# Optimization experiments

Hardware: AMD Instinct MI355X
Metric: run time of the kernel (lower is better)

Reference implementation:

```python
import jax, jax.numpy as jnp
import numpy as np

B, D, N, M = 32, 512, 1024, 1024

def setup_inputs() -> dict:
    key = jax.random.key(0)
    k1, k2 = jax.random.split(key)
    embedding_1 = jax.random.normal(k1, (B, D, N), dtype=jnp.float32)
    embedding_2 = jax.random.normal(k2, (B, D, M), dtype=jnp.float32)
    return {"embedding_1": embedding_1, "embedding_2": embedding_2}

def reference(embedding_1, embedding_2):
    # att[b, n, m] = sum_d e1[b, d, n] * e2[b, d, m]   (bmm of e1^T with e2)
    att = jnp.einsum('bdn,bdm->bnm', embedding_1, embedding_2)
    # double max-pool: max over m then over n -> global max of score matrix
    s = jnp.max(att, axis=(-1, -2))  # [B]
    return s[:, None]  # [B, 1]
```

## Files before the change

### kernel.cpp

```cpp
#include <hip/hip_runtime.h>
#include <hip/hip_bf16.h>

#define B_ 32
#define D_ 512
#define N_ 1024
#define M_ 1024
#define BT 256
#define BK 64
#define NSTEP (D_ / BK)

typedef __attribute__((ext_vector_type(8))) short bf16x8;
typedef __attribute__((ext_vector_type(4))) short s16x4;
typedef __attribute__((ext_vector_type(4))) float f32x4;
typedef __attribute__((ext_vector_type(4))) int   i32x4;
typedef unsigned short ushort_t;

__device__ __forceinline__ unsigned map_f(float f) {
    unsigned b = __float_as_uint(f);
    return (b & 0x80000000u) ? ~b : (b | 0x80000000u);
}

struct __align__(16) GSmem {
    ushort_t As[2][BT * BK];
    ushort_t Bs[2][BT * BK];
    float red[8];
};

__device__ __forceinline__ void load_tile(const float* __restrict__ p, int k0,
                                          int krb, int gr, float4* fl) {
    #pragma unroll
    for (int it = 0; it < 4; ++it) {
        const float* q = p + (size_t)(k0 + krb + it) * N_ + gr * 8;
        fl[2 * it]     = *reinterpret_cast<const float4*>(q);
        fl[2 * it + 1] = *reinterpret_cast<const float4*>(q + 4);
    }
}

__device__ __forceinline__ void flush_tile(char* lds, int krb, int gr, const float4* fl) {
    #pragma unroll
    for (int it = 0; it < 4; ++it) {
        const int k = krb + it;
        const float4& f0 = fl[2 * it];
        const float4& f1 = fl[2 * it + 1];
        __hip_bfloat162 h0 = __float22bfloat162_rn(make_float2(f0.x, f0.y));
        __hip_bfloat162 h1 = __float22bfloat162_rn(make_float2(f0.z, f0.w));
        __hip_bfloat162 h2 = __float22bfloat162_rn(make_float2(f1.x, f1.y));
        __hip_bfloat162 h3 = __float22bfloat162_rn(make_float2(f1.z, f1.w));
        i32x4 v = { *reinterpret_cast<const int*>(&h0), *reinterpret_cast<const int*>(&h1),
                    *reinterpret_cast<const int*>(&h2), *reinterpret_cast<const int*>(&h3) };
        *reinterpret_cast<i32x4*>(lds + k * 512 + 16 * (gr ^ (2 * (k & 3)))) = v;
    }
}

__global__ __launch_bounds__(512, 2)
void fused_gemm_max_kernel(const float* __restrict__ e1, const float* __restrict__ e2,
                           float* __restrict__ out) {
    __shared__ GSmem sm;
    const int wg  = blockIdx.x;
    const int swz = (wg & 7) * 64 + (wg >> 3);
    const int b    = swz >> 4;
    const int tile = swz & 15;
    const int tn = (tile >> 2) * BT;
    const int tc = (tile & 3) * BT;

    const int t    = threadIdx.x;
    const int lane = t & 63;
    const int wave = t >> 6;
    const int wrow = (wave >> 2) * 128;
    const int wcol = (wave & 3) * 64;

    const int krb = (t >> 5) * 4;
    const int gr  = t & 31;

    const int c = lane & 15, g = lane >> 4;
    const int r = c >> 2, d = (c >> 1) & 1, h = c & 1;

    unsigned tbA[8], tbB[4];
    #pragma unroll
    for (int m = 0; m < 8; ++m)
        tbA[m] = (unsigned)((8 * g + r) * 512
               + 16 * ((((wrow >> 3) + 2 * m + d) ^ (2 * r))) + 8 * h);
    #pragma unroll
    for (int n = 0; n < 4; ++n)
        tbB[n] = (unsigned)(65536 + (8 * g + r) * 512
               + 16 * ((((wcol >> 3) + 2 * n + d) ^ (2 * r))) + 8 * h);
    const unsigned ldsbase = (unsigned)(uintptr_t)&sm.As[0][0];

    const float* Ap = e1 + (size_t)b * D_ * N_ + tn;
    const float* Bp = e2 + (size_t)b * D_ * M_ + tc;

    f32x4 acc[8][4] = {};
    float4 fl[8];

    load_tile(Ap, 0, krb, gr, fl);
    flush_tile((char*)sm.As[0], krb, gr, fl);
    load_tile(Bp, 0, krb, gr, fl);
    flush_tile((char*)sm.Bs[0], krb, gr, fl);
    load_tile(Ap, BK, krb, gr, fl);
    asm volatile("s_waitcnt lgkmcnt(0)" ::: "memory");
    __builtin_amdgcn_s_barrier();

    int cur = 0;
    #pragma unroll 1
    for (int ks = 0; ks < NSTEP; ++ks) {
        const unsigned off = ldsbase + (unsigned)cur * 32768u;
        const bool has_next = (ks < NSTEP - 1);

        #pragma unroll
        for (int kk = 0; kk < 2; ++kk) {
            s16x4 alo[8], ahi[8], blo[4], bhi[4];
            #pragma unroll
            for (int m = 0; m < 8; ++m) {
                asm volatile("ds_read_b64_tr_b16 %0, %1 offset:%2"
                             : "=v"(alo[m]) : "v"(tbA[m] + off), "n"(kk * 16384));
                asm volatile("ds_read_b64_tr_b16 %0, %1 offset:%2"
                             : "=v"(ahi[m]) : "v"(tbA[m] + off), "n"(kk * 16384 + 2048));
            }
            #pragma unroll
            for (int n = 0; n < 4; ++n) {
                asm volatile("ds_read_b64_tr_b16 %0, %1 offset:%2"
                             : "=v"(blo[n]) : "v"(tbB[n] + off), "n"(kk * 16384));
                asm volatile("ds_read_b64_tr_b16 %0, %1 offset:%2"
                             : "=v"(bhi[n]) : "v"(tbB[n] + off), "n"(kk * 16384 + 2048));
            }
            asm volatile("s_waitcnt lgkmcnt(0)" ::: "memory");
            __builtin_amdgcn_sched_barrier(0);
            bf16x8 af[8], bf[4];
            #pragma unroll
            for (int m = 0; m < 8; ++m)
                af[m] = __builtin_shufflevector(alo[m], ahi[m], 0, 1, 2, 3, 4, 5, 6, 7);
            #pragma unroll
            for (int n = 0; n < 4; ++n)
                bf[n] = __builtin_shufflevector(blo[n], bhi[n], 0, 1, 2, 3, 4, 5, 6, 7);
            __builtin_amdgcn_s_setprio(1);
            #pragma unroll
            for (int m = 0; m < 8; ++m)
                #pragma unroll
                for (int n = 0; n < 4; ++n)
                    acc[m][n] = __builtin_amdgcn_mfma_f32_16x16x32_bf16(
                        af[m], bf[n], acc[m][n], 0, 0, 0);
            __builtin_amdgcn_s_setprio(0);

            if (kk == 0 && has_next) {
                flush_tile((char*)sm.As[cur ^ 1], krb, gr, fl);
                load_tile(Bp, (ks + 1) * BK, krb, gr, fl);
            }
        }
        if (has_next) {
            flush_tile((char*)sm.Bs[cur ^ 1], krb, gr, fl);
            if (ks < NSTEP - 2)
                load_tile(Ap, (ks + 2) * BK, krb, gr, fl);
        }
        asm volatile("s_waitcnt lgkmcnt(0)" ::: "memory");
        __builtin_amdgcn_s_barrier();
        cur ^= 1;
    }

    float tmax = acc[0][0][0];
    #pragma unroll
    for (int m = 0; m < 8; ++m)
        #pragma unroll
        for (int n = 0; n < 4; ++n)
            #pragma unroll
            for (int i = 0; i < 4; ++i)
                tmax = fmaxf(tmax, acc[m][n][i]);
    #pragma unroll
    for (int off2 = 32; off2; off2 >>= 1)
        tmax = fmaxf(tmax, __shfl_xor(tmax, off2));
    if (lane == 0) sm.red[wave] = tmax;
    __syncthreads();
    if (t == 0) {
        float m8 = sm.red[0];
        #pragma unroll
        for (int w = 1; w < 8; ++w) m8 = fmaxf(m8, sm.red[w]);
        atomicMax(reinterpret_cast<unsigned*>(out) + b, map_f(m8));
    }
}

__global__ void finalize_kernel(float* out) {
    const int i = threadIdx.x;
    unsigned u = reinterpret_cast<unsigned*>(out)[i];
    out[i] = __uint_as_float((u & 0x80000000u) ? (u ^ 0x80000000u) : ~u);
}

extern "C" void kernel_launch(void* const* d_in, const int* in_sizes, int n_in,
                              void* d_out, int out_size, void* d_ws, size_t ws_size,
                              hipStream_t stream) {
    const float* e1 = (const float*)d_in[0];
    const float* e2 = (const float*)d_in[1];
    float* out = (float*)d_out;

    (void)hipMemsetAsync(d_out, 0, B_ * sizeof(float), stream);

    fused_gemm_max_kernel<<<dim3(512), 512, 0, stream>>>(e1, e2, out);
    finalize_kernel<<<1, B_, 0, stream>>>(out);
}
```

Measured before the change: 52.70 us.

## Software-pipeline LDS transpose reads with MFMA using partial lgkmcnt waits

Splits each K-step's fragment loads into half-tiles and issues the next half's ds_read_b64_tr_b16 reads before running the MFMAs on the current half. Partial s_waitcnt lgkmcnt counts replace the full drain, so LDS read latency can overlap matrix-core work. The A/B tile flush and global load are moved to sit between the pipelined stages. The exchange is more live fragment registers and hand-counted wait values, which are fragile: the LDS writes from flush_tile also count toward lgkmcnt.

Result: slower. 55.68 us (+5.6%).

```diff
diff --git a/kernel.cpp b/kernel.cpp
--- a/kernel.cpp
+++ b/kernel.cpp
@@ -52,6 +52,40 @@
     }
 }
 
+#define ISSUE_A(lo, hi, base_m, kkoff)                                          \
+    _Pragma("unroll")                                                           \
+    for (int mm = 0; mm < 4; ++mm) {                                            \
+        asm volatile("ds_read_b64_tr_b16 %0, %1 offset:%2"                      \
+                     : "=v"(lo[mm]) : "v"(tbA[(base_m) + mm] + off), "n"(kkoff));\
+        asm volatile("ds_read_b64_tr_b16 %0, %1 offset:%2"                      \
+                     : "=v"(hi[mm]) : "v"(tbA[(base_m) + mm] + off), "n"((kkoff) + 2048)); \
+    }
+
+#define ISSUE_B(lo, hi, kkoff)                                                  \
+    _Pragma("unroll")                                                           \
+    for (int nn = 0; nn < 4; ++nn) {                                            \
+        asm volatile("ds_read_b64_tr_b16 %0, %1 offset:%2"                      \
+                     : "=v"(lo[nn]) : "v"(tbB[nn] + off), "n"(kkoff));          \
+        asm volatile("ds_read_b64_tr_b16 %0, %1 offset:%2"                      \
+                     : "=v"(hi[nn]) : "v"(tbB[nn] + off), "n"((kkoff) + 2048)); \
+    }
+
+#define MFMA16(alo_, ahi_, bf_, mb)                                             \
+    {                                                                           \
+        bf16x8 af_[4];                                                          \
+        _Pragma("unroll")                                                       \
+        for (int mm = 0; mm < 4; ++mm)                                          \
+            af_[mm] = __builtin_shufflevector(alo_[mm], ahi_[mm], 0,1,2,3,4,5,6,7); \
+        __builtin_amdgcn_s_setprio(1);                                          \
+        _Pragma("unroll")                                                       \
+        for (int mm = 0; mm < 4; ++mm)                                          \
+            _Pragma("unroll")                                                   \
+            for (int nn = 0; nn < 4; ++nn)                                      \
+                acc[(mb) + mm][nn] = __builtin_amdgcn_mfma_f32_16x16x32_bf16(   \
+                    af_[mm], bf_[nn], acc[(mb) + mm][nn], 0, 0, 0);             \
+        __builtin_amdgcn_s_setprio(0);                                          \
+    }
+
 __global__ __launch_bounds__(512, 2)
 void fused_gemm_max_kernel(const float* __restrict__ e1, const float* __restrict__ e2,
                            float* __restrict__ out) {
@@ -106,46 +140,46 @@
         const unsigned off = ldsbase + (unsigned)cur * 32768u;
         const bool has_next = (ks < NSTEP - 1);
 
-        #pragma unroll
-        for (int kk = 0; kk < 2; ++kk) {
-            s16x4 alo[8], ahi[8], blo[4], bhi[4];
-            #pragma unroll
-            for (int m = 0; m < 8; ++m) {
-                asm volatile("ds_read_b64_tr_b16 %0, %1 offset:%2"
-                             : "=v"(alo[m]) : "v"(tbA[m] + off), "n"(kk * 16384));
-                asm volatile("ds_read_b64_tr_b16 %0, %1 offset:%2"
-                             : "=v"(ahi[m]) : "v"(tbA[m] + off), "n"(kk * 16384 + 2048));
-            }
-            #pragma unroll
-            for (int n = 0; n < 4; ++n) {
-                asm volatile("ds_read_b64_tr_b16 %0, %1 offset:%2"
-                             : "=v"(blo[n]) : "v"(tbB[n] + off), "n"(kk * 16384));
-                asm volatile("ds_read_b64_tr_b16 %0, %1 offset:%2"
-                             : "=v"(bhi[n]) : "v"(tbB[n] + off), "n"(kk * 16384 + 2048));
-            }
+        s16x4 a0lo[4], a0hi[4], a1lo[4], a1hi[4];
+        s16x4 b0lo[4], b0hi[4], b1lo[4], b1hi[4];
+
+        ISSUE_A(a0lo, a0hi, 0, 0)
+        ISSUE_B(b0lo, b0hi, 0)
+
+        ISSUE_A(a1lo, a1hi, 4, 0)
+        asm volatile("s_waitcnt lgkmcnt(8)" ::: "memory");
+        __builtin_amdgcn_sched_barrier(0);
+        bf16x8 bf0[4];
+        #pragma unroll
+        for (int nn = 0; nn < 4; ++nn)
+            bf0[nn] = __builtin_shufflevector(b0lo[nn], b0hi[nn], 0,1,2,3,4,5,6,7);
+        MFMA16(a0lo, a0hi, bf0, 0)
+
+        asm volatile("s_waitcnt lgkmcnt(0)" ::: "memory");
+        __builtin_amdgcn_sched_barrier(0);
+        ISSUE_A(a0lo, a0hi, 0, 16384)
+        MFMA16(a1lo, a1hi, bf0, 4)
+
+        ISSUE_B(b1lo, b1hi, 16384)
+        ISSUE_A(a1lo, a1hi, 4, 16384)
+        if (has_next) {
+            flush_tile((char*)sm.As[cur ^ 1], krb, gr, fl);
+            load_tile(Bp, (ks + 1) * BK, krb, gr, fl);
+        }
+        asm volatile("s_waitcnt lgkmcnt(12)" ::: "memory");
+        __builtin_amdgcn_sched_barrier(0);
+        bf16x8 bf1[4];
+        #pragma unroll
+        for (int nn = 0; nn < 4; ++nn)
+            bf1[nn] = __builtin_shufflevector(b1lo[nn], b1hi[nn], 0,1,2,3,4,5,6,7);
+        MFMA16(a0lo, a0hi, bf1, 0)
+
+        if (has_next)
+            asm volatile("s_waitcnt lgkmcnt(4)" ::: "memory");
+        else
             asm volatile("s_waitcnt lgkmcnt(0)" ::: "memory");
-            __builtin_amdgcn_sched_barrier(0);
-            bf16x8 af[8], bf[4];
-            #pragma unroll
-            for (int m = 0; m < 8; ++m)
-                af[m] = __builtin_shufflevector(alo[m], ahi[m], 0, 1, 2, 3, 4, 5, 6, 7);
-            #pragma unroll
-            for (int n = 0; n < 4; ++n)
-                bf[n] = __builtin_shufflevector(blo[n], bhi[n], 0, 1, 2, 3, 4, 5, 6, 7);
-            __builtin_amdgcn_s_setprio(1);
-            #pragma unroll
-            for (int m = 0; m < 8; ++m)
-                #pragma unroll
-                for (int n = 0; n < 4; ++n)
-                    acc[m][n] = __builtin_amdgcn_mfma_f32_16x16x32_bf16(
-                        af[m], bf[n], acc[m][n], 0, 0, 0);
-            __builtin_amdgcn_s_setprio(0);
-
-            if (kk == 0 && has_next) {
-                flush_tile((char*)sm.As[cur ^ 1], krb, gr, fl);
-                load_tile(Bp, (ks + 1) * BK, krb, gr, fl);
-            }
-        }
+        __builtin_amdgcn_sched_barrier(0);
+        MFMA16(a1lo, a1hi, bf1, 4)
         if (has_next) {
             flush_tile((char*)sm.Bs[cur ^ 1], krb, gr, fl);
             if (ks < NSTEP - 2)
```

## Process two column tiles per workgroup and halve the grid

Applied to the files above, without the earlier changes.

Each workgroup now computes two adjacent 256x256 output tiles in sequence, continuing the pipelined K loop across both. A partial max is taken and the accumulators are reset at the midpoint. The grid drops from 512 to 256 workgroups, which removes the tail effect and amortises the prologue and epilogue. The A tile is still reloaded from global memory for the second tile, so there is no A reuse, and fewer workgroups means less parallelism across the 256 CUs.

Result: faster. 50.99 us, median of 2 (-3.3%).

```diff
diff --git a/kernel.cpp b/kernel.cpp
--- a/kernel.cpp
+++ b/kernel.cpp
@@ -7,7 +7,7 @@
 #define M_ 1024
 #define BT 256
 #define BK 64
-#define NSTEP (D_ / BK)
+#define NIT 16
 
 typedef __attribute__((ext_vector_type(8))) short bf16x8;
 typedef __attribute__((ext_vector_type(4))) short s16x4;
@@ -57,11 +57,11 @@
                            float* __restrict__ out) {
     __shared__ GSmem sm;
     const int wg  = blockIdx.x;
-    const int swz = (wg & 7) * 64 + (wg >> 3);
-    const int b    = swz >> 4;
-    const int tile = swz & 15;
-    const int tn = (tile >> 2) * BT;
-    const int tc = (tile & 3) * BT;
+    const int swz = (wg & 7) * 32 + (wg >> 3);
+    const int b    = swz >> 3;
+    const int pair = swz & 7;
+    const int tn  = (pair >> 1) * BT;
+    const int tc0 = (pair & 1) * 512;
 
     const int t    = threadIdx.x;
     const int lane = t & 63;
@@ -86,15 +86,17 @@
                + 16 * ((((wcol >> 3) + 2 * n + d) ^ (2 * r))) + 8 * h);
     const unsigned ldsbase = (unsigned)(uintptr_t)&sm.As[0][0];
 
-    const float* Ap = e1 + (size_t)b * D_ * N_ + tn;
-    const float* Bp = e2 + (size_t)b * D_ * M_ + tc;
+    const float* Ap  = e1 + (size_t)b * D_ * N_ + tn;
+    const float* Bp0 = e2 + (size_t)b * D_ * M_ + tc0;
+    const float* Bp1 = Bp0 + BT;
 
     f32x4 acc[8][4] = {};
     float4 fl[8];
+    float tmax = -3.4e38f;
 
     load_tile(Ap, 0, krb, gr, fl);
     flush_tile((char*)sm.As[0], krb, gr, fl);
-    load_tile(Bp, 0, krb, gr, fl);
+    load_tile(Bp0, 0, krb, gr, fl);
     flush_tile((char*)sm.Bs[0], krb, gr, fl);
     load_tile(Ap, BK, krb, gr, fl);
     asm volatile("s_waitcnt lgkmcnt(0)" ::: "memory");
@@ -102,9 +104,9 @@
 
     int cur = 0;
     #pragma unroll 1
-    for (int ks = 0; ks < NSTEP; ++ks) {
+    for (int it = 0; it < NIT; ++it) {
         const unsigned off = ldsbase + (unsigned)cur * 32768u;
-        const bool has_next = (ks < NSTEP - 1);
+        const bool has_next = (it < NIT - 1);
 
         #pragma unroll
         for (int kk = 0; kk < 2; ++kk) {
@@ -143,20 +145,33 @@
 
             if (kk == 0 && has_next) {
                 flush_tile((char*)sm.As[cur ^ 1], krb, gr, fl);
-                load_tile(Bp, (ks + 1) * BK, krb, gr, fl);
+                const float* bp = (it + 1 < 8) ? Bp0 : Bp1;
+                load_tile(bp, ((it + 1) & 7) * BK, krb, gr, fl);
             }
         }
+
+        if (it == 7) {
+            #pragma unroll
+            for (int m = 0; m < 8; ++m)
+                #pragma unroll
+                for (int n = 0; n < 4; ++n) {
+                    #pragma unroll
+                    for (int i = 0; i < 4; ++i)
+                        tmax = fmaxf(tmax, acc[m][n][i]);
+                    acc[m][n] = f32x4{0.f, 0.f, 0.f, 0.f};
+                }
+        }
+
         if (has_next) {
             flush_tile((char*)sm.Bs[cur ^ 1], krb, gr, fl);
-            if (ks < NSTEP - 2)
-                load_tile(Ap, (ks + 2) * BK, krb, gr, fl);
+            if (it < NIT - 2)
+                load_tile(Ap, ((it + 2) & 7) * BK, krb, gr, fl);
         }
         asm volatile("s_waitcnt lgkmcnt(0)" ::: "memory");
         __builtin_amdgcn_s_barrier();
         cur ^= 1;
     }
 
-    float tmax = acc[0][0][0];
     #pragma unroll
     for (int m = 0; m < 8; ++m)
         #pragma unroll
@@ -192,6 +207,6 @@
 
     (void)hipMemsetAsync(d_out, 0, B_ * sizeof(float), stream);
 
-    fused_gemm_max_kernel<<<dim3(512), 512, 0, stream>>>(e1, e2, out);
+    fused_gemm_max_kernel<<<dim3(256), 512, 0, stream>>>(e1, e2, out);
     finalize_kernel<<<1, B_, 0, stream>>>(out);
 }
```
